# Performance work log

Hardware: AMD Instinct MI355X
Metric: run time of the kernel (lower is better)

Reference implementation:

```python
import jax, jax.numpy as jnp
import numpy as np

SEGMENT_LENGTHS = (2048, 4096, 8192)
DILATION_RATES = (1, 2, 4)
NUM_HEADS = 12
EMBED_DIM = 768
B, N = 2, 8192


def setup_inputs() -> dict:
    key = jax.random.key(0)
    ks = jax.random.split(key, 11)
    E = EMBED_DIM
    return {
        "query": jax.random.normal(ks[0], (B, N, E), jnp.float32),
        "key": jax.random.normal(ks[1], (B, N, E), jnp.float32),
        "value": jax.random.normal(ks[2], (B, N, E), jnp.float32),
        "Wq": jax.random.normal(ks[3], (E, E), jnp.float32) * (E ** -0.5),
        "bq": jax.random.normal(ks[4], (E,), jnp.float32) * 0.02,
        "Wk": jax.random.normal(ks[5], (E, E), jnp.float32) * (E ** -0.5),
        "bk": jax.random.normal(ks[6], (E,), jnp.float32) * 0.02,
        "Wv": jax.random.normal(ks[7], (E, E), jnp.float32) * (E ** -0.5),
        "bv": jax.random.normal(ks[8], (E,), jnp.float32) * 0.02,
        "Wo": jax.random.normal(ks[9], (E, E), jnp.float32) * (E ** -0.5),
        "bo": jax.random.normal(ks[10], (E,), jnp.float32) * 0.02,
    }


def _dilated_attention(q, k, v):
    # q, k, v: [b, n, h, d]
    b, n, h, d = q.shape
    num_groups = len(DILATION_RATES)
    g = h // num_groups  # heads per dilation group
    scale = float(1.0 / np.sqrt(d))  # xformers default softmax scale
    out = jnp.zeros_like(q)
    for i, (r, s) in enumerate(zip(DILATION_RATES, SEGMENT_LENGTHS)):
        off = i % r
        hmin, hmax = i * g, (i + 1) * g
        nseg = n // s
        # gather: [b, nseg, s/r, g, d]
        qg = q.reshape(b, nseg, s, h, d)[:, :, off::r, hmin:hmax, :]
        kg = k.reshape(b, nseg, s, h, d)[:, :, off::r, hmin:hmax, :]
        vg = v.reshape(b, nseg, s, h, d)[:, :, off::r, hmin:hmax, :]
        scores = jnp.einsum("bnqhd,bnkhd->bnhqk", qg, kg) * scale
        attn = jax.nn.softmax(scores, axis=-1)
        x = jnp.einsum("bnhqk,bnkhd->bnqhd", attn, vg)
        out = (
            out.reshape(b, nseg, s, h, d)
            .at[:, :, off::r, hmin:hmax, :]
            .add(x)
            .reshape(b, n, h, d)
        )
    # faithful to original: normalize by sum over the sequence dimension
    return out / jnp.sum(out, axis=1, keepdims=True)


def reference(query, key, value, Wq, bq, Wk, bk, Wv, bv, Wo, bo):
    b, n, e = query.shape
    h = NUM_HEADS
    d = e // h
    q = (query @ Wq.T + bq).reshape(b, n, h, d)
    k = (key @ Wk.T + bk).reshape(b, n, h, d)
    v = (value @ Wv.T + bv).reshape(b, n, h, d)
    x = _dilated_attention(q, k, v)
    x = x.reshape(b, n, e)
    return x @ Wo.T + bo
```

## Files before the change

### kernel.cpp

```cpp
#include <hip/hip_runtime.h>
#include <hip/hip_bf16.h>
#include <cmath>
#include <cstdint>

#define B_ 2
#define N_ 8192
#define H_ 12
#define D_ 64
#define E_ 768
#define M_ (B_*N_)

typedef __attribute__((ext_vector_type(8))) short short8;
typedef __attribute__((ext_vector_type(4))) short short4v;
typedef __attribute__((ext_vector_type(4))) float float4v;

__device__ inline short f2b(float f) {
  union { float f; unsigned u; } x; x.f = f;
  unsigned r = (x.u + 0x7fffu + ((x.u >> 16) & 1u)) >> 16;
  return (short)r;
}
__device__ inline float b2f(short s) {
  union { unsigned u; float f; } x; x.u = ((unsigned)(unsigned short)s) << 16;
  return x.f;
}
__device__ inline void split2(float f, short& h, short& l) {
  h = f2b(f);
  l = f2b(f - b2f(h));
}
__device__ inline unsigned pack_trunc(float a, float b) {
  return (__float_as_uint(b) & 0xffff0000u) | (__float_as_uint(a) >> 16);
}

#define MFMA(a, b, c) __builtin_amdgcn_mfma_f32_16x16x32_bf16((a), (b), (c), 0, 0, 0)

#define GLOAD_LDS16(g, l) \
  __builtin_amdgcn_global_load_lds((const __attribute__((address_space(1))) void*)(g), \
      (__attribute__((address_space(3))) void*)(l), 16, 0, 0)

__global__ __launch_bounds__(256) void split_kernel(const float* __restrict__ src,
    short* __restrict__ hi, short* __restrict__ lo, int count4)
{
  int i = blockIdx.x * 256 + threadIdx.x;
  if (i >= count4) return;
  float4v t = ((const float4v*)src)[i];
  short4v h4, l4; short hh, ll;
  split2(t.x, hh, ll); h4.x = hh; l4.x = ll;
  split2(t.y, hh, ll); h4.y = hh; l4.y = ll;
  split2(t.z, hh, ll); h4.z = hh; l4.z = ll;
  split2(t.w, hh, ll); h4.w = hh; l4.w = ll;
  ((short4v*)hi)[i] = h4;
  ((short4v*)lo)[i] = l4;
}

__global__ __launch_bounds__(256) void split_w4(
    const float* __restrict__ w0, const float* __restrict__ w1,
    const float* __restrict__ w2, const float* __restrict__ w3,
    short* __restrict__ planes)
{
  int which = blockIdx.y;
  const float* src = which == 0 ? w0 : which == 1 ? w1 : which == 2 ? w2 : w3;
  short* hi = planes + (size_t)(2 * which) * (E_ * E_);
  short* lo = planes + (size_t)(2 * which + 1) * (E_ * E_);
  int i = blockIdx.x * 256 + threadIdx.x;
  if (i >= E_ * E_ / 4) return;
  float4v t = ((const float4v*)src)[i];
  short4v h4, l4; short hh, ll;
  split2(t.x, hh, ll); h4.x = hh; l4.x = ll;
  split2(t.y, hh, ll); h4.y = hh; l4.y = ll;
  split2(t.z, hh, ll); h4.z = hh; l4.z = ll;
  split2(t.w, hh, ll); h4.w = hh; l4.w = ll;
  ((short4v*)hi)[i] = h4;
  ((short4v*)lo)[i] = l4;
}

__global__ __launch_bounds__(256) void inv_kernel(const float* __restrict__ sums,
    float* __restrict__ inv)
{
  int i = blockIdx.x * 256 + threadIdx.x;
  if (i < B_ * E_) inv[i] = 1.0f / sums[i];
}

__global__ __launch_bounds__(256) void prep_out(const float* __restrict__ attn,
    const float* __restrict__ inv, short* __restrict__ xnh, short* __restrict__ xnl)
{
  size_t e4 = ((size_t)blockIdx.x * 256 + threadIdx.x) * 4;
  int e = (int)(e4 % E_);
  int b = (int)(e4 / ((size_t)E_ * N_));
  float4v a = *(const float4v*)(attn + e4);
  float4v iv = *(const float4v*)(inv + (size_t)b * E_ + e);
  a *= iv;
  short4v h4, l4; short hh, ll;
  split2(a.x, hh, ll); h4.x = hh; l4.x = ll;
  split2(a.y, hh, ll); h4.y = hh; l4.y = ll;
  split2(a.z, hh, ll); h4.z = hh; l4.z = ll;
  split2(a.w, hh, ll); h4.w = hh; l4.w = ll;
  *(short4v*)&xnh[e4] = h4;
  *(short4v*)&xnl[e4] = l4;
}

template<bool OUT_PAIR>
__global__ __launch_bounds__(256) void gemm_dma(
    const short* __restrict__ Ah, const short* __restrict__ Al,
    const short* __restrict__ Wh, const short* __restrict__ Wl,
    const float* __restrict__ bias, void* __restrict__ OutH, short* __restrict__ OutL)
{
  __shared__ short Ash[4096], Asl[4096], Wsh[4096], Wsl[4096];
  const int tid = threadIdx.x;
  const int m0 = blockIdx.y * 128;
  const int n0 = blockIdx.x * 128;
  const int w = tid >> 6, lane = tid & 63, quad = lane >> 4, l16 = lane & 15;
  const int wr = w >> 1, wc = w & 1;
  const int cq = (l16 >> 1) & 3;
  const int dmarow = lane >> 2;
  const int dmacc = (((lane & 3) ^ ((lane >> 3) & 3))) * 8;

  float4v acc[4][4];
#pragma unroll
  for (int a = 0; a < 4; ++a)
#pragma unroll
    for (int c = 0; c < 4; ++c) acc[a][c] = (float4v)0.0f;

  for (int kt = 0; kt < 24; ++kt) {
    const int k0 = kt * 32;
#pragma unroll
    for (int i = 0; i < 2; ++i) {
      int c = w * 2 + i;
      int ldso = c * 512 + lane * 8;
      size_t ga = (size_t)(m0 + c * 16 + dmarow) * E_ + k0 + dmacc;
      size_t gw = (size_t)(n0 + c * 16 + dmarow) * E_ + k0 + dmacc;
      GLOAD_LDS16(Ah + ga, &Ash[ldso]);
      GLOAD_LDS16(Al + ga, &Asl[ldso]);
      GLOAD_LDS16(Wh + gw, &Wsh[ldso]);
      GLOAD_LDS16(Wl + gw, &Wsl[ldso]);
    }
    __syncthreads();

    short8 afh[4], afl[4], bfh[4], bfl[4];
#pragma unroll
    for (int rt = 0; rt < 4; ++rt) {
      int ao = (wr * 64 + rt * 16 + l16) * 32 + (quad ^ cq) * 8;
      afh[rt] = *(const short8*)&Ash[ao];
      afl[rt] = *(const short8*)&Asl[ao];
      int wo = (wc * 64 + rt * 16 + l16) * 32 + (quad ^ cq) * 8;
      bfh[rt] = *(const short8*)&Wsh[wo];
      bfl[rt] = *(const short8*)&Wsl[wo];
    }
#pragma unroll
    for (int rt = 0; rt < 4; ++rt)
#pragma unroll
      for (int ct = 0; ct < 4; ++ct) {
        float4v a = acc[rt][ct];
        a = MFMA(afh[rt], bfh[ct], a);
        a = MFMA(afh[rt], bfl[ct], a);
        a = MFMA(afl[rt], bfh[ct], a);
        acc[rt][ct] = a;
      }
    __syncthreads();
  }

#pragma unroll
  for (int ct = 0; ct < 4; ++ct) {
    int n = n0 + wc * 64 + ct * 16 + l16;
    float bv = bias[n];
#pragma unroll
    for (int rt = 0; rt < 4; ++rt) {
#pragma unroll
      for (int i = 0; i < 4; ++i) {
        int m = m0 + wr * 64 + rt * 16 + quad * 4 + i;
        float v = acc[rt][ct][i] + bv;
        if constexpr (OUT_PAIR) {
          short hh, ll; split2(v, hh, ll);
          ((short*)OutH)[(size_t)m * E_ + n] = hh;
          OutL[(size_t)m * E_ + n] = ll;
        } else {
          ((float*)OutH)[(size_t)m * E_ + n] = v;
        }
      }
    }
  }
}

__device__ __host__ inline int hoff_of(int g, int hg) {
  return g == 0 ? hg * 8192 : (g == 1 ? 32768 + hg * 4096 : 49152 + hg * 2048);
}

__global__ __launch_bounds__(256) void transpose_v(const short* __restrict__ vh,
    const short* __restrict__ vl, short* __restrict__ vgh, short* __restrict__ vgl)
{
  __shared__ short Lh[64 * 68], Ll[64 * 68];
  int bid = blockIdx.x;
  int b = 0;
  if (bid >= 896) { b = 1; bid -= 896; }
  int g, hg, tile;
  if (bid < 512)      { g = 0; hg = bid >> 7; tile = bid & 127; }
  else if (bid < 768) { g = 1; hg = (bid - 512) >> 6; tile = (bid - 512) & 63; }
  else                { g = 2; hg = (bid - 768) >> 5; tile = (bid - 768) & 31; }
  const int h = g * 4 + hg, r = 1 << g, off = g;
  const int ext = 8192 >> g;
  const int jj0 = tile * 64, seg = jj0 >> 11, j0 = jj0 & 2047;
  const int n0 = seg * (2048 << g) + off + j0 * r;
  const int tid = threadIdx.x;

#pragma unroll
  for (int p = 0; p < 2; ++p) {
    int c = tid + p * 256;
    int jr = c >> 3, c8 = (c & 7) * 8;
    size_t gsrc = ((size_t)(b * N_ + n0 + jr * r) * H_ + h) * D_ + c8;
    *(short8*)&Lh[jr * 68 + c8] = *(const short8*)(vh + gsrc);
    *(short8*)&Ll[jr * 68 + c8] = *(const short8*)(vl + gsrc);
  }
  __syncthreads();
  size_t basebh = ((size_t)b * 57344 + hoff_of(g, hg)) * 64;
#pragma unroll
  for (int p = 0; p < 2; ++p) {
    int c = tid + p * 256;
    int dd = c >> 3, jc = (c & 7) * 8;
    short8 oh, ol;
#pragma unroll
    for (int u = 0; u < 8; ++u) {
      oh[u] = Lh[(jc + u) * 68 + dd];
      ol[u] = Ll[(jc + u) * 68 + dd];
    }
    size_t gdst = basebh + (size_t)dd * ext + jj0 + jc;
    *(short8*)(vgh + gdst) = oh;
    *(short8*)(vgl + gdst) = ol;
  }
}

__global__ __launch_bounds__(256, 4) void attn_kernel(
    const short* __restrict__ qh, const short* __restrict__ ql,
    const short* __restrict__ kh, const short* __restrict__ kl,
    const short* __restrict__ vgh, const short* __restrict__ vgl,
    float* __restrict__ attn_out, float* __restrict__ sums)
{
  __shared__ __align__(16) short Ksh[2][32 * 72], Ksl[2][32 * 72];
  __shared__ __align__(16) short Vth[2][64 * 40], Vtl[2][64 * 40];

  int bid = blockIdx.x;
  int g, t;
  if (bid < 512)      { g = 0; t = bid; }
  else if (bid < 768) { g = 1; t = bid - 512; }
  else                { g = 2; t = bid - 768; }
  const int qtile = t & 15; t >>= 4;
  const int hg = t & 3; t >>= 2;
  const int nseg = 4 >> g;
  const int seg = t & (nseg - 1);
  const int b = t / nseg;
  const int r = 1 << g;
  const int off = g;
  const int h = g * 4 + hg;
  const int segbase = seg * (2048 << g);
  const int ext = 8192 >> g;

  const int tid = threadIdx.x;
  const int w = tid >> 6, lane = tid & 63, quad = lane >> 4, l16 = lane & 15;
  const bool hi5 = (lane & 32) != 0;
  const int addrA = (l16 + ((lane >> 4) & 1) * 32) << 2;
  const int addrB = addrA + 64;

  const size_t vbase = ((size_t)b * 57344 + hoff_of(g, hg)) * 64 + (size_t)seg * 2048;

  if (g > 0) {
#pragma unroll
    for (int res0 = 1; res0 < 4; ++res0) {
      if (res0 >= r) break;
      int res = (off + res0) & (r - 1);
      for (int c = 0; c < 8; ++c) {
        int idx = tid + c * 256;
        int jl = idx >> 4, d0 = (idx & 15) * 4;
        int pos = segbase + res + (qtile * 128 + jl) * r;
        *(float4v*)(attn_out + ((size_t)(b * N_ + pos) * H_ + h) * D_ + d0) = (float4v)0.f;
      }
    }
  }

  short8 qfh[2][2], qfl[2][2];
#pragma unroll
  for (int qt = 0; qt < 2; ++qt) {
    int j = qtile * 128 + w * 32 + qt * 16 + l16;
    int pos = segbase + off + j * r;
    size_t base = ((size_t)(b * N_ + pos) * H_ + h) * D_;
#pragma unroll
    for (int ks = 0; ks < 2; ++ks) {
      qfh[qt][ks] = *(const short8*)(qh + base + ks * 32 + quad * 8);
      qfl[qt][ks] = *(const short8*)(ql + base + ks * 32 + quad * 8);
    }
  }

  const int srow = tid >> 3, sc8 = (tid & 7) * 8;
  const int sdd = tid >> 2, skvc = (tid & 3) * 8;
  size_t gbK = ((size_t)(b * N_ + segbase + off + srow * r) * H_ + h) * D_ + sc8;
  const size_t stepK = (size_t)32 * r * (H_ * D_);
  size_t gbV = vbase + (size_t)sdd * ext + skvc;

  short8 rkh, rkl, rvh, rvl;
#define LOADT(tt) do { \
    size_t ka_ = gbK + (size_t)(tt) * stepK; \
    size_t va_ = gbV + (size_t)(tt) * 32; \
    rkh = *(const short8*)(kh + ka_); rkl = *(const short8*)(kl + ka_); \
    rvh = *(const short8*)(vgh + va_); rvl = *(const short8*)(vgl + va_); \
  } while (0)
#define WRITET(cc) do { \
    *(short8*)&Ksh[cc][srow * 72 + sc8] = rkh; \
    *(short8*)&Ksl[cc][srow * 72 + sc8] = rkl; \
    *(short8*)&Vth[cc][sdd * 40 + skvc] = rvh; \
    *(short8*)&Vtl[cc][sdd * 40 + skvc] = rvl; \
  } while (0)

  float4v o[4][2];
  float mrow[2], lrow[2];
#pragma unroll
  for (int dt = 0; dt < 4; ++dt)
#pragma unroll
    for (int qt = 0; qt < 2; ++qt) o[dt][qt] = (float4v)0.0f;
  mrow[0] = mrow[1] = -INFINITY;
  lrow[0] = lrow[1] = 0.f;

  LOADT(0);
  WRITET(0);
  LOADT(1);
  __syncthreads();
  int cur = 0;

  for (int kt = 0; kt < 64; ++kt) {
    WRITET(cur ^ 1);
    LOADT((kt + 2) & 63);

    const short* Kc_h = Ksh[cur]; const short* Kc_l = Ksl[cur];
    const short* Vc_h = Vth[cur]; const short* Vc_l = Vtl[cur];

    float4v sc[2][2];
    __builtin_amdgcn_s_setprio(1);
#pragma unroll
    for (int kvt = 0; kvt < 2; ++kvt) {
      const int kb = (kvt * 16 + l16) * 72 + quad * 8;
      short8 ah0 = *(const short8*)&Kc_h[kb];
      short8 ah1 = *(const short8*)&Kc_h[kb + 32];
      short8 al0 = *(const short8*)&Kc_l[kb];
      short8 al1 = *(const short8*)&Kc_l[kb + 32];
#pragma unroll
      for (int qt = 0; qt < 2; ++qt) {
        float4v a = (float4v)0.0f;
        a = MFMA(ah0, qfh[qt][0], a); a = MFMA(ah1, qfh[qt][1], a);
        a = MFMA(ah0, qfl[qt][0], a); a = MFMA(ah1, qfl[qt][1], a);
        a = MFMA(al0, qfh[qt][0], a); a = MFMA(al1, qfh[qt][1], a);
        sc[qt][kvt] = a * 0.18033688f;
      }
    }
    __builtin_amdgcn_s_setprio(0);

    short8 pfh[2], pfl[2];
#pragma unroll
    for (int qt = 0; qt < 2; ++qt) {
      float mx = fmaxf(fmaxf(fmaxf(sc[qt][0][0], sc[qt][0][1]),
                             fmaxf(sc[qt][0][2], sc[qt][0][3])),
                       fmaxf(fmaxf(sc[qt][1][0], sc[qt][1][1]),
                             fmaxf(sc[qt][1][2], sc[qt][1][3])));
      mx = fmaxf(mx, __shfl_xor(mx, 16, 64));
      mx = fmaxf(mx, __shfl_xor(mx, 32, 64));
      if (__any(mx > mrow[qt])) {
        float mnew = fmaxf(mrow[qt], mx);
        float alpha = exp2f(mrow[qt] - mnew);
        mrow[qt] = mnew;
        lrow[qt] *= alpha;
#pragma unroll
        for (int dt = 0; dt < 4; ++dt) o[dt][qt] *= alpha;
      }
      float rs = 0.f;
#pragma unroll
      for (int kvt = 0; kvt < 2; ++kvt)
#pragma unroll
        for (int i = 0; i < 4; ++i) {
          float p = exp2f(sc[qt][kvt][i] - mrow[qt]);
          sc[qt][kvt][i] = p;
          rs += p;
        }
      rs += __shfl_xor(rs, 16, 64);
      rs += __shfl_xor(rs, 32, 64);
      lrow[qt] += rs;

      unsigned wv_h[2][2], wv_l[2][2];
#pragma unroll
      for (int kvt = 0; kvt < 2; ++kvt)
#pragma unroll
        for (int c = 0; c < 2; ++c) {
          float pa = sc[qt][kvt][2 * c], pb = sc[qt][kvt][2 * c + 1];
          unsigned ua = __float_as_uint(pa), ub = __float_as_uint(pb);
          wv_h[kvt][c] = (ub & 0xffff0000u) | (ua >> 16);
          float la = pa - __uint_as_float(ua & 0xffff0000u);
          float lb = pb - __uint_as_float(ub & 0xffff0000u);
          wv_l[kvt][c] = pack_trunc(la, lb);
        }
      union { unsigned u[4]; short8 s; } oh, ol;
#pragma unroll
      for (int j = 0; j < 4; ++j) {
        int ad = (j < 2) ? addrA : addrB;
        int c = j & 1;
        unsigned h0 = (unsigned)__builtin_amdgcn_ds_bpermute(ad, (int)wv_h[0][c]);
        unsigned h1 = (unsigned)__builtin_amdgcn_ds_bpermute(ad, (int)wv_h[1][c]);
        unsigned l0 = (unsigned)__builtin_amdgcn_ds_bpermute(ad, (int)wv_l[0][c]);
        unsigned l1 = (unsigned)__builtin_amdgcn_ds_bpermute(ad, (int)wv_l[1][c]);
        oh.u[j] = hi5 ? h1 : h0;
        ol.u[j] = hi5 ? l1 : l0;
      }
      pfh[qt] = oh.s;
      pfl[qt] = ol.s;
    }

    __builtin_amdgcn_s_setprio(1);
#pragma unroll
    for (int dt = 0; dt < 4; ++dt) {
      const int vo = (dt * 16 + l16) * 40 + quad * 8;
      short8 vfh = *(const short8*)&Vc_h[vo];
      short8 vfl = *(const short8*)&Vc_l[vo];
#pragma unroll
      for (int qt = 0; qt < 2; ++qt) {
        float4v a = o[dt][qt];
        a = MFMA(vfh, pfh[qt], a);
        a = MFMA(vfh, pfl[qt], a);
        a = MFMA(vfl, pfh[qt], a);
        o[dt][qt] = a;
      }
    }
    __builtin_amdgcn_s_setprio(0);

    __syncthreads();
    cur ^= 1;
  }
#undef LOADT
#undef WRITET

  float4v sacc[4];
#pragma unroll
  for (int dt = 0; dt < 4; ++dt) sacc[dt] = (float4v)0.0f;
#pragma unroll
  for (int qt = 0; qt < 2; ++qt) {
    float inv_l = 1.0f / lrow[qt];
    int j = qtile * 128 + w * 32 + qt * 16 + l16;
    int pos = segbase + off + j * r;
    float* dst = attn_out + ((size_t)(b * N_ + pos) * H_ + h) * D_;
#pragma unroll
    for (int dt = 0; dt < 4; ++dt) {
      float4v v = o[dt][qt] * inv_l;
      *(float4v*)(dst + dt * 16 + quad * 4) = v;
      sacc[dt] += v;
    }
  }
#pragma unroll
  for (int dt = 0; dt < 4; ++dt) {
#pragma unroll
    for (int i = 0; i < 4; ++i) {
      float x = sacc[dt][i];
      x += __shfl_xor(x, 1, 64);
      x += __shfl_xor(x, 2, 64);
      x += __shfl_xor(x, 4, 64);
      x += __shfl_xor(x, 8, 64);
      if (l16 == 0)
        atomicAdd(&sums[(size_t)b * E_ + h * D_ + dt * 16 + quad * 4 + i], x);
    }
  }
}

extern "C" void kernel_launch(void* const* d_in, const int* in_sizes, int n_in,
                              void* d_out, int out_size, void* d_ws, size_t ws_size,
                              hipStream_t stream)
{
  const float* query = (const float*)d_in[0];
  const float* key_  = (const float*)d_in[1];
  const float* value = (const float*)d_in[2];
  const float* Wq = (const float*)d_in[3];
  const float* bq = (const float*)d_in[4];
  const float* Wk = (const float*)d_in[5];
  const float* bk = (const float*)d_in[6];
  const float* Wv = (const float*)d_in[7];
  const float* bv = (const float*)d_in[8];
  const float* Wo = (const float*)d_in[9];
  const float* bo = (const float*)d_in[10];

  char* ws = (char*)d_ws;
  const size_t szbf = (size_t)M_ * E_ * 2;
  const size_t szvg = (size_t)2 * 57344 * 64 * 2;
  const size_t szw  = (size_t)E_ * E_ * 2;
  short* qh_ = (short*)(ws);
  short* ql_ = (short*)(ws + 1 * szbf);
  short* kh_ = (short*)(ws + 2 * szbf);
  short* kl_ = (short*)(ws + 3 * szbf);
  short* vh_ = (short*)(ws + 4 * szbf);
  short* vl_ = (short*)(ws + 5 * szbf);
  short* ish = (short*)(ws + 6 * szbf);
  short* isl = (short*)(ws + 7 * szbf);
  short* vgh = (short*)(ws + 6 * szbf);
  short* vgl = (short*)(ws + 6 * szbf + szvg);
  short* wsp = (short*)(ws + 8 * szbf);
  float* sums = (float*)(ws + 8 * szbf + 8 * szw);
  float* attn = (float*)(ws + 4 * szbf);
  float* inv  = (float*)qh_;
  short* xnh = kh_;
  short* xnl = kl_;
  short* wqh = wsp + 0 * (szw / 2), *wql = wsp + 1 * (szw / 2);
  short* wkh = wsp + 2 * (szw / 2), *wkl = wsp + 3 * (szw / 2);
  short* wvh = wsp + 4 * (szw / 2), *wvl = wsp + 5 * (szw / 2);
  short* woh = wsp + 6 * (szw / 2), *wol = wsp + 7 * (szw / 2);

  hipMemsetAsync(sums, 0, (size_t)B_ * E_ * sizeof(float), stream);

  split_w4<<<dim3(576, 4), 256, 0, stream>>>(Wq, Wk, Wv, Wo, wsp);

  const int ac4 = M_ * E_ / 4;
  dim3 gg(6, 128), gb(256);
  split_kernel<<<12288, 256, 0, stream>>>(query, ish, isl, ac4);
  gemm_dma<true><<<gg, gb, 0, stream>>>(ish, isl, wqh, wql, bq, qh_, ql_);
  split_kernel<<<12288, 256, 0, stream>>>(key_, ish, isl, ac4);
  gemm_dma<true><<<gg, gb, 0, stream>>>(ish, isl, wkh, wkl, bk, kh_, kl_);
  split_kernel<<<12288, 256, 0, stream>>>(value, ish, isl, ac4);
  gemm_dma<true><<<gg, gb, 0, stream>>>(ish, isl, wvh, wvl, bv, vh_, vl_);

  transpose_v<<<1792, 256, 0, stream>>>(vh_, vl_, vgh, vgl);
  attn_kernel<<<896, 256, 0, stream>>>(qh_, ql_, kh_, kl_, vgh, vgl, attn, sums);
  inv_kernel<<<6, 256, 0, stream>>>(sums, inv);
  prep_out<<<12288, 256, 0, stream>>>(attn, inv, xnh, xnl);
  gemm_dma<false><<<gg, gb, 0, stream>>>(xnh, xnl, woh, wol, bo, d_out, nullptr);
}
```

Measured before the change: 879.2 us.

## Use 16x16x16 MFMA for PV to drop bpermute, fold scale into Q, lazy rescale

The P·V product now uses 16x16x16 bf16 MFMA on short4 fragments, which matches the score accumulator layout directly and removes the ds_bpermute shuffles and the row-sum shuffles in the inner loop. The row sum is reduced across lanes only once at the end. The softmax scale (with log2e) is folded into the Q projection epilogue. The max rescale runs only when the new max exceeds the old by more than 8 (lazy rescaling). Blocks are also remapped so the three dilation groups interleave across the grid. The trade-off is twice as many smaller MFMA instructions for PV, and unnormalized exponentials that can grow up to 2^8 before a rescale.

```diff
diff --git a/kernel.cpp b/kernel.cpp
--- a/kernel.cpp
+++ b/kernel.cpp
@@ -32,6 +32,20 @@
 }
 
 #define MFMA(a, b, c) __builtin_amdgcn_mfma_f32_16x16x32_bf16((a), (b), (c), 0, 0, 0)
+
+#if __has_builtin(__builtin_amdgcn_mfma_f32_16x16x16_bf16)
+#define MFMA16(a, b, c) __builtin_amdgcn_mfma_f32_16x16x16_bf16((a), (b), (c), 0, 0, 0)
+#elif __has_builtin(__builtin_amdgcn_mfma_f32_16x16x16bf16_1k)
+#define MFMA16(a, b, c) __builtin_amdgcn_mfma_f32_16x16x16bf16_1k((a), (b), (c), 0, 0, 0)
+#else
+__device__ inline float4v mfma16_asm(short4v a, short4v b, float4v c) {
+  float4v d = c;
+  asm volatile("v_mfma_f32_16x16x16_bf16 %0, %1, %2, %0"
+               : "+v"(d) : "v"(a), "v"(b));
+  return d;
+}
+#define MFMA16(a, b, c) mfma16_asm((a), (b), (c))
+#endif
 
 #define GLOAD_LDS16(g, l) \
   __builtin_amdgcn_global_load_lds((const __attribute__((address_space(1))) void*)(g), \
@@ -102,7 +116,8 @@
 __global__ __launch_bounds__(256) void gemm_dma(
     const short* __restrict__ Ah, const short* __restrict__ Al,
     const short* __restrict__ Wh, const short* __restrict__ Wl,
-    const float* __restrict__ bias, void* __restrict__ OutH, short* __restrict__ OutL)
+    const float* __restrict__ bias, void* __restrict__ OutH, short* __restrict__ OutL,
+    float oscale)
 {
   __shared__ short Ash[4096], Asl[4096], Wsh[4096], Wsl[4096];
   const int tid = threadIdx.x;
@@ -167,7 +182,7 @@
 #pragma unroll
       for (int i = 0; i < 4; ++i) {
         int m = m0 + wr * 64 + rt * 16 + quad * 4 + i;
-        float v = acc[rt][ct][i] + bv;
+        float v = (acc[rt][ct][i] + bv) * oscale;
         if constexpr (OUT_PAIR) {
           short hh, ll; split2(v, hh, ll);
           ((short*)OutH)[(size_t)m * E_ + n] = hh;
@@ -236,7 +251,7 @@
   __shared__ __align__(16) short Ksh[2][32 * 72], Ksl[2][32 * 72];
   __shared__ __align__(16) short Vth[2][64 * 40], Vtl[2][64 * 40];
 
-  int bid = blockIdx.x;
+  int bid = (blockIdx.x & 7) * 112 + (blockIdx.x >> 3);
   int g, t;
   if (bid < 512)      { g = 0; t = bid; }
   else if (bid < 768) { g = 1; t = bid - 512; }
@@ -254,9 +269,6 @@
 
   const int tid = threadIdx.x;
   const int w = tid >> 6, lane = tid & 63, quad = lane >> 4, l16 = lane & 15;
-  const bool hi5 = (lane & 32) != 0;
-  const int addrA = (l16 + ((lane >> 4) & 1) * 32) << 2;
-  const int addrB = addrA + 64;
 
   const size_t vbase = ((size_t)b * 57344 + hoff_of(g, hg)) * 64 + (size_t)seg * 2048;
 
@@ -344,12 +356,12 @@
         a = MFMA(ah0, qfh[qt][0], a); a = MFMA(ah1, qfh[qt][1], a);
         a = MFMA(ah0, qfl[qt][0], a); a = MFMA(ah1, qfl[qt][1], a);
         a = MFMA(al0, qfh[qt][0], a); a = MFMA(al1, qfh[qt][1], a);
-        sc[qt][kvt] = a * 0.18033688f;
+        sc[qt][kvt] = a;
       }
     }
     __builtin_amdgcn_s_setprio(0);
 
-    short8 pfh[2], pfl[2];
+    short4v pfh[2][2], pfl[2][2];
 #pragma unroll
     for (int qt = 0; qt < 2; ++qt) {
       float mx = fmaxf(fmaxf(fmaxf(sc[qt][0][0], sc[qt][0][1]),
@@ -358,7 +370,7 @@
                              fmaxf(sc[qt][1][2], sc[qt][1][3])));
       mx = fmaxf(mx, __shfl_xor(mx, 16, 64));
       mx = fmaxf(mx, __shfl_xor(mx, 32, 64));
-      if (__any(mx > mrow[qt])) {
+      if (__any(mx > mrow[qt] + 8.0f)) {
         float mnew = fmaxf(mrow[qt], mx);
         float alpha = exp2f(mrow[qt] - mnew);
         mrow[qt] = mnew;
@@ -368,58 +380,43 @@
       }
       float rs = 0.f;
 #pragma unroll
-      for (int kvt = 0; kvt < 2; ++kvt)
-#pragma unroll
-        for (int i = 0; i < 4; ++i) {
-          float p = exp2f(sc[qt][kvt][i] - mrow[qt]);
-          sc[qt][kvt][i] = p;
-          rs += p;
+      for (int kvt = 0; kvt < 2; ++kvt) {
+        float p0 = exp2f(sc[qt][kvt][0] - mrow[qt]);
+        float p1 = exp2f(sc[qt][kvt][1] - mrow[qt]);
+        float p2 = exp2f(sc[qt][kvt][2] - mrow[qt]);
+        float p3 = exp2f(sc[qt][kvt][3] - mrow[qt]);
+        rs += (p0 + p1) + (p2 + p3);
+        union { unsigned u[2]; short4v s; } ph, pl;
+        ph.u[0] = pack_trunc(p0, p1);
+        ph.u[1] = pack_trunc(p2, p3);
+        float l0 = p0 - __uint_as_float(__float_as_uint(p0) & 0xffff0000u);
+        float l1 = p1 - __uint_as_float(__float_as_uint(p1) & 0xffff0000u);
+        float l2 = p2 - __uint_as_float(__float_as_uint(p2) & 0xffff0000u);
+        float l3 = p3 - __uint_as_float(__float_as_uint(p3) & 0xffff0000u);
+        pl.u[0] = pack_trunc(l0, l1);
+        pl.u[1] = pack_trunc(l2, l3);
+        pfh[qt][kvt] = ph.s;
+        pfl[qt][kvt] = pl.s;
+      }
+      lrow[qt] += rs;
+    }
+
+    __builtin_amdgcn_s_setprio(1);
+#pragma unroll
+    for (int dt = 0; dt < 4; ++dt) {
+#pragma unroll
+      for (int kvt = 0; kvt < 2; ++kvt) {
+        const int vo = (dt * 16 + l16) * 40 + kvt * 16 + quad * 4;
+        short4v vfh = *(const short4v*)&Vc_h[vo];
+        short4v vfl = *(const short4v*)&Vc_l[vo];
+#pragma unroll
+        for (int qt = 0; qt < 2; ++qt) {
+          float4v a = o[dt][qt];
+          a = MFMA16(vfh, pfh[qt][kvt], a);
+          a = MFMA16(vfh, pfl[qt][kvt], a);
+          a = MFMA16(vfl, pfh[qt][kvt], a);
+          o[dt][qt] = a;
         }
-      rs += __shfl_xor(rs, 16, 64);
-      rs += __shfl_xor(rs, 32, 64);
-      lrow[qt] += rs;
-
-      unsigned wv_h[2][2], wv_l[2][2];
-#pragma unroll
-      for (int kvt = 0; kvt < 2; ++kvt)
-#pragma unroll
-        for (int c = 0; c < 2; ++c) {
-          float pa = sc[qt][kvt][2 * c], pb = sc[qt][kvt][2 * c + 1];
-          unsigned ua = __float_as_uint(pa), ub = __float_as_uint(pb);
-          wv_h[kvt][c] = (ub & 0xffff0000u) | (ua >> 16);
-          float la = pa - __uint_as_float(ua & 0xffff0000u);
-          float lb = pb - __uint_as_float(ub & 0xffff0000u);
-          wv_l[kvt][c] = pack_trunc(la, lb);
-        }
-      union { unsigned u[4]; short8 s; } oh, ol;
-#pragma unroll
-      for (int j = 0; j < 4; ++j) {
-        int ad = (j < 2) ? addrA : addrB;
-        int c = j & 1;
-        unsigned h0 = (unsigned)__builtin_amdgcn_ds_bpermute(ad, (int)wv_h[0][c]);
-        unsigned h1 = (unsigned)__builtin_amdgcn_ds_bpermute(ad, (int)wv_h[1][c]);
-        unsigned l0 = (unsigned)__builtin_amdgcn_ds_bpermute(ad, (int)wv_l[0][c]);
-        unsigned l1 = (unsigned)__builtin_amdgcn_ds_bpermute(ad, (int)wv_l[1][c]);
-        oh.u[j] = hi5 ? h1 : h0;
-        ol.u[j] = hi5 ? l1 : l0;
-      }
-      pfh[qt] = oh.s;
-      pfl[qt] = ol.s;
-    }
-
-    __builtin_amdgcn_s_setprio(1);
-#pragma unroll
-    for (int dt = 0; dt < 4; ++dt) {
-      const int vo = (dt * 16 + l16) * 40 + quad * 8;
-      short8 vfh = *(const short8*)&Vc_h[vo];
-      short8 vfl = *(const short8*)&Vc_l[vo];
-#pragma unroll
-      for (int qt = 0; qt < 2; ++qt) {
-        float4v a = o[dt][qt];
-        a = MFMA(vfh, pfh[qt], a);
-        a = MFMA(vfh, pfl[qt], a);
-        a = MFMA(vfl, pfh[qt], a);
-        o[dt][qt] = a;
       }
     }
     __builtin_amdgcn_s_setprio(0);
@@ -435,6 +432,8 @@
   for (int dt = 0; dt < 4; ++dt) sacc[dt] = (float4v)0.0f;
 #pragma unroll
   for (int qt = 0; qt < 2; ++qt) {
+    lrow[qt] += __shfl_xor(lrow[qt], 16, 64);
+    lrow[qt] += __shfl_xor(lrow[qt], 32, 64);
     float inv_l = 1.0f / lrow[qt];
     int j = qtile * 128 + w * 32 + qt * 16 + l16;
     int pos = segbase + off + j * r;
@@ -508,16 +507,17 @@
 
   const int ac4 = M_ * E_ / 4;
   dim3 gg(6, 128), gb(256);
+  const float qscale = 0.18033688f;
   split_kernel<<<12288, 256, 0, stream>>>(query, ish, isl, ac4);
-  gemm_dma<true><<<gg, gb, 0, stream>>>(ish, isl, wqh, wql, bq, qh_, ql_);
+  gemm_dma<true><<<gg, gb, 0, stream>>>(ish, isl, wqh, wql, bq, qh_, ql_, qscale);
   split_kernel<<<12288, 256, 0, stream>>>(key_, ish, isl, ac4);
-  gemm_dma<true><<<gg, gb, 0, stream>>>(ish, isl, wkh, wkl, bk, kh_, kl_);
+  gemm_dma<true><<<gg, gb, 0, stream>>>(ish, isl, wkh, wkl, bk, kh_, kl_, 1.0f);
   split_kernel<<<12288, 256, 0, stream>>>(value, ish, isl, ac4);
-  gemm_dma<true><<<gg, gb, 0, stream>>>(ish, isl, wvh, wvl, bv, vh_, vl_);
+  gemm_dma<true><<<gg, gb, 0, stream>>>(ish, isl, wvh, wvl, bv, vh_, vl_, 1.0f);
 
   transpose_v<<<1792, 256, 0, stream>>>(vh_, vl_, vgh, vgl);
   attn_kernel<<<896, 256, 0, stream>>>(qh_, ql_, kh_, kl_, vgh, vgl, attn, sums);
   inv_kernel<<<6, 256, 0, stream>>>(sums, inv);
   prep_out<<<12288, 256, 0, stream>>>(attn, inv, xnh, xnl);
-  gemm_dma<false><<<gg, gb, 0, stream>>>(xnh, xnl, woh, wol, bo, d_out, nullptr);
-}
+  gemm_dma<false><<<gg, gb, 0, stream>>>(xnh, xnl, woh, wol, bo, d_out, nullptr, 1.0f);
+}
```

Result: faster. 850.6 us (-3.3%).
